# Performance work log

Measured on AMD Instinct MI355X. Metric: run time of the kernel, lower is better.

The kernel has to match this reference:

```python
import jax, jax.numpy as jnp
import numpy as np

N, NFEAT, NHID, NCLASS = 8192, 512, 256, 2
ALPHA = 0.5


def setup_inputs() -> dict:
    key = jax.random.key(0)
    k1, k2, k3, k4, k5 = jax.random.split(key, 5)
    x = jax.random.normal(k1, (N, NFEAT), dtype=jnp.float32)
    adj = jax.random.uniform(k2, (N, N), dtype=jnp.float32)
    # GraphConvolution init: uniform(-stdv, stdv), stdv = 1/sqrt(out_features)
    s1 = 1.0 / np.sqrt(NHID)
    W1 = jax.random.uniform(k3, (NFEAT, NHID), dtype=jnp.float32, minval=-s1, maxval=s1)
    s2 = 1.0 / np.sqrt(NCLASS)
    W2 = jax.random.uniform(k4, (NHID, NCLASS), dtype=jnp.float32, minval=-s2, maxval=s2)
    b2 = jax.random.uniform(k5, (NCLASS,), dtype=jnp.float32, minval=-s2, maxval=s2)
    return {"x": x, "adj": adj, "W1": W1, "W2": W2, "b2": b2}


def _mid_filter_2(adj, alpha):
    # D_row = diag(rowsum^-0.5), D_col = diag(colsum^-0.5); inf -> 0
    d_row = jnp.power(jnp.sum(adj, axis=1), -0.5)
    d_row = jnp.where(jnp.isinf(d_row), 0.0, d_row)
    d_col = jnp.power(jnp.sum(adj, axis=0), -0.5)
    d_col = jnp.where(jnp.isinf(d_col), 0.0, d_col)
    # (adj @ D_col)^T @ D_row)^T == d_row[:,None] * adj * d_col[None,:]
    DAD = d_row[:, None] * adj * d_col[None, :]
    I = jnp.eye(adj.shape[0], dtype=adj.dtype)
    return jnp.matmul(alpha * I - DAD, I + DAD)


def reference(x, adj, W1, W2, b2):
    adj_f = _mid_filter_2(adj, ALPHA)
    # hidden layer (no bias): relu(adj_f @ (x @ W1)); dropout = identity (eval)
    h = jax.nn.relu(jnp.matmul(adj_f, jnp.matmul(x, W1)))
    # output layer (with bias)
    out = jnp.matmul(adj_f, jnp.matmul(h, W2)) + b2
    return jax.nn.log_softmax(out, axis=-1)
```

## Files before the change

kernel.cpp:

```cpp
#include <hip/hip_runtime.h>
#include <hip/hip_bf16.h>

typedef unsigned short u16;
typedef unsigned int u32;
typedef __attribute__((ext_vector_type(8))) short short8;
typedef __attribute__((ext_vector_type(4))) float f32x4;

#define NN 8192
#define NF 512
#define NH 256
#define SPLITZ 4
#define RB 256

__device__ __forceinline__ float bf2f(u32 u) {
  union { u32 i; float f; } v; v.i = u << 16; return v.f;
}
__device__ __forceinline__ u16 f2bf(float f) {
  union { __hip_bfloat16 b; u16 u; } v; v.b = __float2bfloat16(f); return v.u;
}
__device__ __forceinline__ u32 pack2(float a, float b) {
  return (u32)f2bf(a) | ((u32)f2bf(b) << 16);
}

__global__ __launch_bounds__(256) void conv_adj_k(const float* __restrict__ adj,
                                                  u16* __restrict__ adjb,
                                                  float* __restrict__ rowsum_part,
                                                  float* __restrict__ colsum_part) {
  __shared__ float red[4][32];
  const int t = threadIdx.x;
  const int w = t >> 6, lane = t & 63;
  const int s = blockIdx.x;
  const int c0 = s * 2048 + t * 8;
  const int r0 = blockIdx.y * 32;
  float cp[8] = {0.f, 0.f, 0.f, 0.f, 0.f, 0.f, 0.f, 0.f};
  for (int r = 0; r < 32; ++r) {
    const size_t base = (size_t)(r0 + r) * NN + c0;
    float4 v0 = *(const float4*)(adj + base);
    float4 v1 = *(const float4*)(adj + base + 4);
    uint4 pk;
    pk.x = pack2(v0.x, v0.y); pk.y = pack2(v0.z, v0.w);
    pk.z = pack2(v1.x, v1.y); pk.w = pack2(v1.z, v1.w);
    *(uint4*)(adjb + base) = pk;
    cp[0] += v0.x; cp[1] += v0.y; cp[2] += v0.z; cp[3] += v0.w;
    cp[4] += v1.x; cp[5] += v1.y; cp[6] += v1.z; cp[7] += v1.w;
    float rs = (v0.x + v0.y) + (v0.z + v0.w) + ((v1.x + v1.y) + (v1.z + v1.w));
#pragma unroll
    for (int off = 32; off > 0; off >>= 1) rs += __shfl_down(rs, off, 64);
    if (lane == 0) red[w][r] = rs;
  }
  __syncthreads();
  if (t < 32)
    rowsum_part[(size_t)s * NN + r0 + t] =
        (red[0][t] + red[1][t]) + (red[2][t] + red[3][t]);
  float* cdst = colsum_part + (size_t)blockIdx.y * NN + c0;
  *(float4*)cdst = make_float4(cp[0], cp[1], cp[2], cp[3]);
  *(float4*)(cdst + 4) = make_float4(cp[4], cp[5], cp[6], cp[7]);
}

__global__ __launch_bounds__(256) void reduce_sums_k(const float* __restrict__ rowp,
                                                     const float* __restrict__ colp,
                                                     float* __restrict__ drow,
                                                     float* __restrict__ dcol) {
  const int i = blockIdx.x * 256 + threadIdx.x;
  const float rs = (rowp[i] + rowp[NN + i]) + (rowp[2 * NN + i] + rowp[3 * NN + i]);
  drow[i] = (rs > 0.f) ? rsqrtf(rs) : 0.f;
  float cs = 0.f;
#pragma unroll 8
  for (int rb = 0; rb < RB; ++rb) cs += colp[(size_t)rb * NN + i];
  dcol[i] = (cs > 0.f) ? rsqrtf(cs) : 0.f;
}

__global__ __launch_bounds__(256) void convx_k(const float* __restrict__ x,
                                               u16* __restrict__ xb) {
  const size_t i = ((size_t)blockIdx.x * 256 + threadIdx.x) * 8;
  float4 v0 = *(const float4*)(x + i);
  float4 v1 = *(const float4*)(x + i + 4);
  uint4 pk;
  pk.x = pack2(v0.x, v0.y); pk.y = pack2(v0.z, v0.w);
  pk.z = pack2(v1.x, v1.y); pk.w = pack2(v1.z, v1.w);
  *(uint4*)(xb + i) = pk;
}

__global__ __launch_bounds__(256) void convw1_k(const float* __restrict__ in,
                                                u16* __restrict__ out) {
  __shared__ float tile[32][33];
  const int tx = threadIdx.x & 31, ty = threadIdx.x >> 5;
  const int c0 = blockIdx.x * 32;
  const int r0 = blockIdx.y * 32;
#pragma unroll
  for (int d = 0; d < 32; d += 8)
    tile[ty + d][tx] = in[(size_t)(r0 + ty + d) * NH + c0 + tx];
  __syncthreads();
#pragma unroll
  for (int d = 0; d < 32; d += 8)
    out[(size_t)(c0 + ty + d) * NF + r0 + tx] = f2bf(tile[tx][ty + d]);
}

__device__ __forceinline__ void stage128(const u16* __restrict__ A, int lda,
                                         const u16* __restrict__ Bt, int ldb,
                                         int m0, int n0, int kk,
                                         u16* as_, u16* bs_, int tid) {
#pragma unroll
  for (int h = 0; h < 2; ++h) {
    const int slot = tid + h * 256;
    const int row = slot >> 2, kc = slot & 3;
    const u16* srcA = A + (size_t)(m0 + row) * lda + kk + kc * 8;
    __builtin_amdgcn_global_load_lds((const __attribute__((address_space(1))) void*)srcA,
                                     (__attribute__((address_space(3))) void*)(as_ + slot * 8),
                                     16, 0, 0);
    const u16* srcB = Bt + (size_t)(n0 + row) * ldb + kk + kc * 8;
    __builtin_amdgcn_global_load_lds((const __attribute__((address_space(1))) void*)srcB,
                                     (__attribute__((address_space(3))) void*)(bs_ + slot * 8),
                                     16, 0, 0);
  }
}

__global__ __launch_bounds__(256) void gemm_k(const u16* __restrict__ A, int lda,
                                              const u16* __restrict__ Bt, int ldb,
                                              int kChunk, float* __restrict__ out) {
  __shared__ __align__(16) u16 As[2][128 * 32];
  __shared__ __align__(16) u16 Bs[2][128 * 32];
  const int tid = threadIdx.x;
  const int w = tid >> 6, lane = tid & 63;
  const int lq = lane >> 4, lr = lane & 15;
  const int wr = (w >> 1) * 64, wc = (w & 1) * 64;
  const int n0 = blockIdx.x * 128;
  const int m0 = blockIdx.y * 128;
  const int kk0 = blockIdx.z * kChunk;
  const int nk = kChunk >> 5;

  f32x4 acc[4][4] = {};

  stage128(A, lda, Bt, ldb, m0, n0, kk0, As[0], Bs[0], tid);
  for (int kt = 0; kt < nk; ++kt) {
    const int cur = kt & 1;
    __syncthreads();
    if (kt + 1 < nk)
      stage128(A, lda, Bt, ldb, m0, n0, kk0 + ((kt + 1) << 5), As[cur ^ 1], Bs[cur ^ 1], tid);
    short8 a[4], b[4];
#pragma unroll
    for (int i = 0; i < 4; ++i)
      a[i] = *(const short8*)(As[cur] + (wr + i * 16 + lr) * 32 + lq * 8);
#pragma unroll
    for (int i = 0; i < 4; ++i)
      b[i] = *(const short8*)(Bs[cur] + (wc + i * 16 + lr) * 32 + lq * 8);
#pragma unroll
    for (int i = 0; i < 4; ++i)
#pragma unroll
      for (int j = 0; j < 4; ++j)
        acc[i][j] = __builtin_amdgcn_mfma_f32_16x16x32_bf16(a[i], b[j], acc[i][j], 0, 0, 0);
  }

  float* o = out + (size_t)blockIdx.z * ((size_t)NN * NH);
#pragma unroll
  for (int i = 0; i < 4; ++i)
#pragma unroll
    for (int j = 0; j < 4; ++j) {
      const int gn = n0 + wc + j * 16 + lr;
      const int gm0 = m0 + wr + i * 16 + lq * 4;
#pragma unroll
      for (int r = 0; r < 4; ++r)
        o[(size_t)(gm0 + r) * NH + gn] = acc[i][j][r];
    }
}

__global__ __launch_bounds__(256) void t1_k(const float* __restrict__ P,
                                            const float* __restrict__ dcol,
                                            u16* __restrict__ B1t) {
  __shared__ float tile[32][33];
  const int tx = threadIdx.x & 31, ty = threadIdx.x >> 5;
  const int c0 = blockIdx.x * 32;
  const int r0 = blockIdx.y * 32;
#pragma unroll
  for (int d = 0; d < 32; d += 8) {
    const int rr = r0 + ty + d;
    tile[ty + d][tx] = dcol[rr] * P[(size_t)rr * NH + c0 + tx];
  }
  __syncthreads();
#pragma unroll
  for (int d = 0; d < 32; d += 8)
    B1t[(size_t)(c0 + ty + d) * NN + r0 + tx] = f2bf(tile[tx][ty + d]);
}

__global__ __launch_bounds__(256) void r2_k(const float* __restrict__ Qp,
                                            const float* __restrict__ drow,
                                            const float* __restrict__ dcol,
                                            float* __restrict__ Q1,
                                            u16* __restrict__ B2t) {
  __shared__ float tile[32][33];
  const int tx = threadIdx.x & 31, ty = threadIdx.x >> 5;
  const int c0 = blockIdx.x * 32;
  const int r0 = blockIdx.y * 32;
  const size_t sl = (size_t)NN * NH;
#pragma unroll
  for (int d = 0; d < 32; d += 8) {
    const int rr = r0 + ty + d;
    const size_t idx = (size_t)rr * NH + c0 + tx;
    const float s = (Qp[idx] + Qp[idx + sl]) + (Qp[idx + 2 * sl] + Qp[idx + 3 * sl]);
    const float q = drow[rr] * s;
    Q1[idx] = q;
    tile[ty + d][tx] = dcol[rr] * q;
  }
  __syncthreads();
#pragma unroll
  for (int d = 0; d < 32; d += 8)
    B2t[(size_t)(c0 + ty + d) * NN + r0 + tx] = f2bf(tile[tx][ty + d]);
}

__global__ __launch_bounds__(256) void r3_k(const float* __restrict__ Hp,
                                            const float* __restrict__ P,
                                            const float* __restrict__ Q1,
                                            const float* __restrict__ drow,
                                            u16* __restrict__ Hb) {
  const size_t i = ((size_t)blockIdx.x * 256 + threadIdx.x) * 4;
  const int row = (int)(i >> 8);
  const size_t sl = (size_t)NN * NH;
  float4 a = *(const float4*)(Hp + i);
  float4 b = *(const float4*)(Hp + i + sl);
  float4 c = *(const float4*)(Hp + i + 2 * sl);
  float4 d = *(const float4*)(Hp + i + 3 * sl);
  float4 p = *(const float4*)(P + i);
  float4 q = *(const float4*)(Q1 + i);
  const float dr = drow[row];
  const float h0 = fmaxf(0.5f * p.x - 0.5f * q.x - dr * ((a.x + b.x) + (c.x + d.x)), 0.f);
  const float h1 = fmaxf(0.5f * p.y - 0.5f * q.y - dr * ((a.y + b.y) + (c.y + d.y)), 0.f);
  const float h2 = fmaxf(0.5f * p.z - 0.5f * q.z - dr * ((a.z + b.z) + (c.z + d.z)), 0.f);
  const float h3 = fmaxf(0.5f * p.w - 0.5f * q.w - dr * ((a.w + b.w) + (c.w + d.w)), 0.f);
  uint2 pk;
  pk.x = pack2(h0, h1);
  pk.y = pack2(h2, h3);
  *(uint2*)(Hb + i) = pk;
}

__global__ __launch_bounds__(256) void r_k(const u16* __restrict__ H,
                                           const float* __restrict__ W2,
                                           const float* __restrict__ dcol,
                                           float* __restrict__ R, float* __restrict__ B3) {
  const int w = threadIdx.x >> 6, lane = threadIdx.x & 63;
  const int i = blockIdx.x * 4 + w;
  uint2 hv = *(const uint2*)(H + (size_t)i * NH + lane * 4);
  float4 w01 = *(const float4*)(W2 + lane * 8);
  float4 w23 = *(const float4*)(W2 + lane * 8 + 4);
  const float h0 = bf2f(hv.x & 0xffffu), h1 = bf2f(hv.x >> 16);
  const float h2 = bf2f(hv.y & 0xffffu), h3 = bf2f(hv.y >> 16);
  float a0 = h0 * w01.x + h1 * w01.z + h2 * w23.x + h3 * w23.z;
  float a1 = h0 * w01.y + h1 * w01.w + h2 * w23.y + h3 * w23.w;
#pragma unroll
  for (int off = 32; off > 0; off >>= 1) {
    a0 += __shfl_down(a0, off, 64);
    a1 += __shfl_down(a1, off, 64);
  }
  if (lane == 0) {
    R[i * 2] = a0;
    R[i * 2 + 1] = a1;
    const float dc = dcol[i];
    B3[i * 2] = dc * a0;
    B3[i * 2 + 1] = dc * a1;
  }
}

__global__ __launch_bounds__(256) void gemv_k(
    const u16* __restrict__ adjb, const float* __restrict__ B,
    const float* __restrict__ drow, const float* __restrict__ dcol,
    const float* __restrict__ Rin, const float* __restrict__ S1in,
    const float* __restrict__ b2, float* __restrict__ S1out,
    float* __restrict__ B4, float* __restrict__ outp, int mode) {
  const int i = blockIdx.x;
  const int t = threadIdx.x;
  float a0 = 0.f, a1 = 0.f;
#pragma unroll
  for (int c = 0; c < 4; ++c) {
    const int col = c * 2048 + t * 8;
    uint4 av = *(const uint4*)(adjb + (size_t)i * NN + col);
    const u32* aw = (const u32*)&av;
    float bv[16];
    *(float4*)(bv) = *(const float4*)(B + col * 2);
    *(float4*)(bv + 4) = *(const float4*)(B + col * 2 + 4);
    *(float4*)(bv + 8) = *(const float4*)(B + col * 2 + 8);
    *(float4*)(bv + 12) = *(const float4*)(B + col * 2 + 12);
#pragma unroll
    for (int j = 0; j < 8; ++j) {
      const u32 a = aw[j >> 1];
      const float aval = bf2f((j & 1) ? (a >> 16) : (a & 0xffffu));
      a0 += aval * bv[2 * j];
      a1 += aval * bv[2 * j + 1];
    }
  }
#pragma unroll
  for (int off = 32; off > 0; off >>= 1) {
    a0 += __shfl_down(a0, off, 64);
    a1 += __shfl_down(a1, off, 64);
  }
  __shared__ float red[8];
  const int w = t >> 6, lane = t & 63;
  if (lane == 0) { red[w] = a0; red[4 + w] = a1; }
  __syncthreads();
  if (t == 0) {
    float s0 = (red[0] + red[1]) + (red[2] + red[3]);
    float s1 = (red[4] + red[5]) + (red[6] + red[7]);
    const float dr = drow[i];
    s0 *= dr; s1 *= dr;
    if (mode == 0) {
      S1out[i * 2] = s0;
      S1out[i * 2 + 1] = s1;
      const float dc = dcol[i];
      B4[i * 2] = dc * s0;
      B4[i * 2 + 1] = dc * s1;
    } else {
      const float l0 = 0.5f * Rin[i * 2] - 0.5f * S1in[i * 2] - s0 + b2[0];
      const float l1 = 0.5f * Rin[i * 2 + 1] - 0.5f * S1in[i * 2 + 1] - s1 + b2[1];
      const float m = fmaxf(l0, l1);
      const float lse = m + logf(__expf(l0 - m) + __expf(l1 - m));
      outp[i * 2] = l0 - lse;
      outp[i * 2 + 1] = l1 - lse;
    }
  }
}

extern "C" void kernel_launch(void* const* d_in, const int* in_sizes, int n_in,
                              void* d_out, int out_size, void* d_ws, size_t ws_size,
                              hipStream_t stream) {
  (void)in_sizes; (void)n_in; (void)out_size; (void)ws_size;
  const float* x   = (const float*)d_in[0];
  const float* adj = (const float*)d_in[1];
  const float* W1  = (const float*)d_in[2];
  const float* W2  = (const float*)d_in[3];
  const float* b2  = (const float*)d_in[4];
  float* outp = (float*)d_out;

  char* ws = (char*)d_ws;
  size_t off = 0;
  auto alloc = [&](size_t bytes) -> char* {
    char* p = ws + off;
    off += (bytes + 255) & ~(size_t)255;
    return p;
  };
  u16* adjb  = (u16*)alloc((size_t)NN * NN * 2);
  u16* xb    = (u16*)alloc((size_t)NN * NF * 2);
  u16* W1t   = (u16*)alloc((size_t)NH * NF * 2);
  float* rowp = (float*)alloc((size_t)4 * NN * 4);
  float* colp = (float*)alloc((size_t)RB * NN * 4);
  float* drow = (float*)alloc((size_t)NN * 4);
  float* dcol = (float*)alloc((size_t)NN * 4);
  float* P   = (float*)alloc((size_t)NN * NH * 4);
  u16* B1t   = (u16*)alloc((size_t)NH * NN * 2);
  float* Qp  = (float*)alloc((size_t)SPLITZ * NN * NH * 4);
  float* Q1  = (float*)alloc((size_t)NN * NH * 4);
  u16* B2t   = (u16*)alloc((size_t)NH * NN * 2);
  u16* Hb    = (u16*)alloc((size_t)NN * NH * 2);
  float* R   = (float*)alloc((size_t)NN * 2 * 4);
  float* B3  = (float*)alloc((size_t)NN * 2 * 4);
  float* S1  = (float*)alloc((size_t)NN * 2 * 4);
  float* B4  = (float*)alloc((size_t)NN * 2 * 4);
  float* Hp  = Qp;

  conv_adj_k<<<dim3(4, RB), 256, 0, stream>>>(adj, adjb, rowp, colp);
  reduce_sums_k<<<NN / 256, 256, 0, stream>>>(rowp, colp, drow, dcol);
  convx_k<<<2048, 256, 0, stream>>>(x, xb);
  convw1_k<<<dim3(8, 16), 256, 0, stream>>>(W1, W1t);

  gemm_k<<<dim3(2, 64, 1), 256, 0, stream>>>(xb, NF, W1t, NF, NF, P);
  t1_k<<<dim3(8, 256), 256, 0, stream>>>(P, dcol, B1t);

  gemm_k<<<dim3(2, 64, SPLITZ), 256, 0, stream>>>(adjb, NN, B1t, NN, NN / SPLITZ, Qp);
  r2_k<<<dim3(8, 256), 256, 0, stream>>>(Qp, drow, dcol, Q1, B2t);

  gemm_k<<<dim3(2, 64, SPLITZ), 256, 0, stream>>>(adjb, NN, B2t, NN, NN / SPLITZ, Hp);
  r3_k<<<2048, 256, 0, stream>>>(Hp, P, Q1, drow, Hb);

  r_k<<<NN / 4, 256, 0, stream>>>(Hb, W2, dcol, R, B3);
  gemv_k<<<NN, 256, 0, stream>>>(adjb, B3, drow, dcol, nullptr, nullptr, nullptr, S1, B4, nullptr, 0);
  gemv_k<<<NN, 256, 0, stream>>>(adjb, B4, drow, dcol, R, S1, b2, nullptr, nullptr, outp, 1);
}
```

Baseline: 661.7 us.

## Use 256x256-tile direct-to-LDS GEMM for adjacency products with deeper split-K

Replaces the two large adjacency GEMMs with a new 512-thread kernel whose 256x256 output tile spans the full hidden width. Each block reads its slice of the bf16 adjacency matrix once, instead of once per N-tile as before. The kernel stages A and B straight into double-buffered LDS with global_load_lds and uses 8x4 MFMA accumulators per wave. Split-K goes from 4 to 8 so the grid still fills the GPU, and the reduction kernels now loop over SPLITZ. The cost is twice as much partial-sum traffic, plus heavy LDS usage that limits occupancy and may cause bank conflicts.

```diff
diff --git a/kernel.cpp b/kernel.cpp
--- a/kernel.cpp
+++ b/kernel.cpp
@@ -9,7 +9,7 @@
 #define NN 8192
 #define NF 512
 #define NH 256
-#define SPLITZ 4
+#define SPLITZ 8
 #define RB 256
 
 __device__ __forceinline__ float bf2f(u32 u) {
@@ -164,6 +164,77 @@
     }
 }
 
+__device__ __forceinline__ void stage256(const u16* __restrict__ A, int lda,
+                                         const u16* __restrict__ Bt, int ldb,
+                                         int m0, int kk,
+                                         u16* as_, u16* bs_, int tid) {
+#pragma unroll
+  for (int h = 0; h < 4; ++h) {
+    const int slot = tid + h * 512;
+    const int row = slot >> 3, kc = (slot & 7) * 8;
+    const u16* srcA = A + (size_t)(m0 + row) * lda + kk + kc;
+    __builtin_amdgcn_global_load_lds((const __attribute__((address_space(1))) void*)srcA,
+                                     (__attribute__((address_space(3))) void*)(as_ + slot * 8),
+                                     16, 0, 0);
+    const u16* srcB = Bt + (size_t)row * ldb + kk + kc;
+    __builtin_amdgcn_global_load_lds((const __attribute__((address_space(1))) void*)srcB,
+                                     (__attribute__((address_space(3))) void*)(bs_ + slot * 8),
+                                     16, 0, 0);
+  }
+}
+
+__global__ __launch_bounds__(512, 2) void gemm256_k(const u16* __restrict__ A, int lda,
+                                                    const u16* __restrict__ Bt, int ldb,
+                                                    int kChunk, float* __restrict__ out) {
+  __shared__ __align__(16) u16 As[2][256 * 64];
+  __shared__ __align__(16) u16 Bs[2][256 * 64];
+  const int tid = threadIdx.x;
+  const int w = tid >> 6, lane = tid & 63;
+  const int lq = lane >> 4, lr = lane & 15;
+  const int wr = (w >> 2) * 128;
+  const int wc = (w & 3) * 64;
+  const int m0 = blockIdx.x * 256;
+  const int kk0 = blockIdx.y * kChunk;
+  const int nk = kChunk >> 6;
+
+  f32x4 acc[8][4] = {};
+
+  stage256(A, lda, Bt, ldb, m0, kk0, As[0], Bs[0], tid);
+  for (int kt = 0; kt < nk; ++kt) {
+    const int cur = kt & 1;
+    __syncthreads();
+    if (kt + 1 < nk)
+      stage256(A, lda, Bt, ldb, m0, kk0 + ((kt + 1) << 6), As[cur ^ 1], Bs[cur ^ 1], tid);
+#pragma unroll
+    for (int kk2 = 0; kk2 < 2; ++kk2) {
+      short8 a[8], b[4];
+#pragma unroll
+      for (int i = 0; i < 8; ++i)
+        a[i] = *(const short8*)(As[cur] + (wr + i * 16 + lr) * 64 + kk2 * 32 + lq * 8);
+#pragma unroll
+      for (int j = 0; j < 4; ++j)
+        b[j] = *(const short8*)(Bs[cur] + (wc + j * 16 + lr) * 64 + kk2 * 32 + lq * 8);
+#pragma unroll
+      for (int i = 0; i < 8; ++i)
+#pragma unroll
+        for (int j = 0; j < 4; ++j)
+          acc[i][j] = __builtin_amdgcn_mfma_f32_16x16x32_bf16(a[i], b[j], acc[i][j], 0, 0, 0);
+    }
+  }
+
+  float* o = out + (size_t)blockIdx.y * ((size_t)NN * NH);
+#pragma unroll
+  for (int i = 0; i < 8; ++i)
+#pragma unroll
+    for (int j = 0; j < 4; ++j) {
+      const int gn = wc + j * 16 + lr;
+      const int gm0 = m0 + wr + i * 16 + lq * 4;
+#pragma unroll
+      for (int r = 0; r < 4; ++r)
+        o[(size_t)(gm0 + r) * NH + gn] = acc[i][j][r];
+    }
+}
+
 __global__ __launch_bounds__(256) void t1_k(const float* __restrict__ P,
                                             const float* __restrict__ dcol,
                                             u16* __restrict__ B1t) {
@@ -196,7 +267,9 @@
   for (int d = 0; d < 32; d += 8) {
     const int rr = r0 + ty + d;
     const size_t idx = (size_t)rr * NH + c0 + tx;
-    const float s = (Qp[idx] + Qp[idx + sl]) + (Qp[idx + 2 * sl] + Qp[idx + 3 * sl]);
+    float s = 0.f;
+#pragma unroll
+    for (int z = 0; z < SPLITZ; ++z) s += Qp[idx + (size_t)z * sl];
     const float q = drow[rr] * s;
     Q1[idx] = q;
     tile[ty + d][tx] = dcol[rr] * q;
@@ -215,17 +288,19 @@
   const size_t i = ((size_t)blockIdx.x * 256 + threadIdx.x) * 4;
   const int row = (int)(i >> 8);
   const size_t sl = (size_t)NN * NH;
-  float4 a = *(const float4*)(Hp + i);
-  float4 b = *(const float4*)(Hp + i + sl);
-  float4 c = *(const float4*)(Hp + i + 2 * sl);
-  float4 d = *(const float4*)(Hp + i + 3 * sl);
+  float4 s = make_float4(0.f, 0.f, 0.f, 0.f);
+#pragma unroll
+  for (int z = 0; z < SPLITZ; ++z) {
+    float4 v = *(const float4*)(Hp + i + (size_t)z * sl);
+    s.x += v.x; s.y += v.y; s.z += v.z; s.w += v.w;
+  }
   float4 p = *(const float4*)(P + i);
   float4 q = *(const float4*)(Q1 + i);
   const float dr = drow[row];
-  const float h0 = fmaxf(0.5f * p.x - 0.5f * q.x - dr * ((a.x + b.x) + (c.x + d.x)), 0.f);
-  const float h1 = fmaxf(0.5f * p.y - 0.5f * q.y - dr * ((a.y + b.y) + (c.y + d.y)), 0.f);
-  const float h2 = fmaxf(0.5f * p.z - 0.5f * q.z - dr * ((a.z + b.z) + (c.z + d.z)), 0.f);
-  const float h3 = fmaxf(0.5f * p.w - 0.5f * q.w - dr * ((a.w + b.w) + (c.w + d.w)), 0.f);
+  const float h0 = fmaxf(0.5f * p.x - 0.5f * q.x - dr * s.x, 0.f);
+  const float h1 = fmaxf(0.5f * p.y - 0.5f * q.y - dr * s.y, 0.f);
+  const float h2 = fmaxf(0.5f * p.z - 0.5f * q.z - dr * s.z, 0.f);
+  const float h3 = fmaxf(0.5f * p.w - 0.5f * q.w - dr * s.w, 0.f);
   uint2 pk;
   pk.x = pack2(h0, h1);
   pk.y = pack2(h2, h3);
@@ -362,10 +437,10 @@
   gemm_k<<<dim3(2, 64, 1), 256, 0, stream>>>(xb, NF, W1t, NF, NF, P);
   t1_k<<<dim3(8, 256), 256, 0, stream>>>(P, dcol, B1t);
 
-  gemm_k<<<dim3(2, 64, SPLITZ), 256, 0, stream>>>(adjb, NN, B1t, NN, NN / SPLITZ, Qp);
+  gemm256_k<<<dim3(32, SPLITZ), 512, 0, stream>>>(adjb, NN, B1t, NN, NN / SPLITZ, Qp);
   r2_k<<<dim3(8, 256), 256, 0, stream>>>(Qp, drow, dcol, Q1, B2t);
 
-  gemm_k<<<dim3(2, 64, SPLITZ), 256, 0, stream>>>(adjb, NN, B2t, NN, NN / SPLITZ, Hp);
+  gemm256_k<<<dim3(32, SPLITZ), 512, 0, stream>>>(adjb, NN, B2t, NN, NN / SPLITZ, Hp);
   r3_k<<<2048, 256, 0, stream>>>(Hp, P, Q1, drow, Hb);
 
   r_k<<<NN / 4, 256, 0, stream>>>(Hb, W2, dcol, R, B3);
```

Result: no change. 652.8 us (-1.3%).

## Replace split-K adjacency GEMMs with full-N-width tile kernel and fuse epilogues

Applied to the files above, without the earlier changes.

Replaces the two split-K 8192x8192x256 adjacency GEMMs with a new kernel where each 512-thread block computes a 32x256 output strip over the whole K range. It uses double-buffered XOR-swizzled LDS tiles and applies the drow scaling in the epilogue, so the four-way partial-sum buffers and the reduction kernels r2_k and r3_k go away. The relu/H step is fused into the W2 projection kernel, and the x and W1 conversion kernels are merged into one launch. The risk is only 256 blocks with a small M tile, which may underfill the GPU and reuse adjacency tiles poorly compared with the 128x128 split-K tiling.

```diff
diff --git a/kernel.cpp b/kernel.cpp
--- a/kernel.cpp
+++ b/kernel.cpp
@@ -9,8 +9,8 @@
 #define NN 8192
 #define NF 512
 #define NH 256
-#define SPLITZ 4
 #define RB 256
+#define BKNZ 64
 
 __device__ __forceinline__ float bf2f(u32 u) {
   union { u32 i; float f; } v; v.i = u << 16; return v.f;
@@ -70,30 +70,32 @@
   dcol[i] = (cs > 0.f) ? rsqrtf(cs) : 0.f;
 }
 
-__global__ __launch_bounds__(256) void convx_k(const float* __restrict__ x,
-                                               u16* __restrict__ xb) {
-  const size_t i = ((size_t)blockIdx.x * 256 + threadIdx.x) * 8;
-  float4 v0 = *(const float4*)(x + i);
-  float4 v1 = *(const float4*)(x + i + 4);
-  uint4 pk;
-  pk.x = pack2(v0.x, v0.y); pk.y = pack2(v0.z, v0.w);
-  pk.z = pack2(v1.x, v1.y); pk.w = pack2(v1.z, v1.w);
-  *(uint4*)(xb + i) = pk;
-}
-
-__global__ __launch_bounds__(256) void convw1_k(const float* __restrict__ in,
-                                                u16* __restrict__ out) {
+__global__ __launch_bounds__(256) void convxw1_k(const float* __restrict__ x,
+                                                 u16* __restrict__ xb,
+                                                 const float* __restrict__ W1,
+                                                 u16* __restrict__ W1t) {
   __shared__ float tile[32][33];
-  const int tx = threadIdx.x & 31, ty = threadIdx.x >> 5;
-  const int c0 = blockIdx.x * 32;
-  const int r0 = blockIdx.y * 32;
-#pragma unroll
-  for (int d = 0; d < 32; d += 8)
-    tile[ty + d][tx] = in[(size_t)(r0 + ty + d) * NH + c0 + tx];
-  __syncthreads();
-#pragma unroll
-  for (int d = 0; d < 32; d += 8)
-    out[(size_t)(c0 + ty + d) * NF + r0 + tx] = f2bf(tile[tx][ty + d]);
+  if (blockIdx.x < 2048) {
+    const size_t i = ((size_t)blockIdx.x * 256 + threadIdx.x) * 8;
+    float4 v0 = *(const float4*)(x + i);
+    float4 v1 = *(const float4*)(x + i + 4);
+    uint4 pk;
+    pk.x = pack2(v0.x, v0.y); pk.y = pack2(v0.z, v0.w);
+    pk.z = pack2(v1.x, v1.y); pk.w = pack2(v1.z, v1.w);
+    *(uint4*)(xb + i) = pk;
+  } else {
+    const int blk = blockIdx.x - 2048;
+    const int tx = threadIdx.x & 31, ty = threadIdx.x >> 5;
+    const int c0 = (blk & 7) * 32;
+    const int r0 = (blk >> 3) * 32;
+#pragma unroll
+    for (int d = 0; d < 32; d += 8)
+      tile[ty + d][tx] = W1[(size_t)(r0 + ty + d) * NH + c0 + tx];
+    __syncthreads();
+#pragma unroll
+    for (int d = 0; d < 32; d += 8)
+      W1t[(size_t)(c0 + ty + d) * NF + r0 + tx] = f2bf(tile[tx][ty + d]);
+  }
 }
 
 __device__ __forceinline__ void stage128(const u16* __restrict__ A, int lda,
@@ -164,9 +166,89 @@
     }
 }
 
-__global__ __launch_bounds__(256) void t1_k(const float* __restrict__ P,
+__device__ __forceinline__ void stage_nz(const u16* __restrict__ A,
+                                         const u16* __restrict__ Bt,
+                                         int m0, int kk,
+                                         u16* as_, u16* bs_, int tid) {
+  if (tid < 256) {
+    const int row = tid >> 3, kc = (tid & 7) * 8;
+    const int sc = kc ^ ((row & 7) << 3);
+    const u16* srcA = A + (size_t)(m0 + row) * NN + kk + sc;
+    __builtin_amdgcn_global_load_lds((const __attribute__((address_space(1))) void*)srcA,
+                                     (__attribute__((address_space(3))) void*)(as_ + tid * 8),
+                                     16, 0, 0);
+  }
+#pragma unroll
+  for (int h = 0; h < 4; ++h) {
+    const int slot = tid + h * 512;
+    const int row = slot >> 3, kc = (slot & 7) * 8;
+    const int sc = kc ^ ((row & 7) << 3);
+    const u16* srcB = Bt + (size_t)row * NN + kk + sc;
+    __builtin_amdgcn_global_load_lds((const __attribute__((address_space(1))) void*)srcB,
+                                     (__attribute__((address_space(3))) void*)(bs_ + slot * 8),
+                                     16, 0, 0);
+  }
+}
+
+__global__ __launch_bounds__(512) void gemm_nz_k(const u16* __restrict__ A,
+                                                 const u16* __restrict__ Bt,
+                                                 const float* __restrict__ drow,
+                                                 float* __restrict__ out) {
+  __shared__ __align__(16) u16 As[2][32 * BKNZ];
+  __shared__ __align__(16) u16 Bs[2][256 * BKNZ];
+  const int tid = threadIdx.x;
+  const int w = tid >> 6, lane = tid & 63;
+  const int lq = lane >> 4, lr = lane & 15;
+  const int wc = w * 32;
+  const int m0 = blockIdx.x * 32;
+
+  f32x4 acc[2][2] = {};
+
+  stage_nz(A, Bt, m0, 0, As[0], Bs[0], tid);
+  const int nk = NN / BKNZ;
+  for (int kt = 0; kt < nk; ++kt) {
+    const int cur = kt & 1;
+    __syncthreads();
+    if (kt + 1 < nk)
+      stage_nz(A, Bt, m0, (kt + 1) * BKNZ, As[cur ^ 1], Bs[cur ^ 1], tid);
+#pragma unroll
+    for (int kk2 = 0; kk2 < BKNZ / 32; ++kk2) {
+      short8 a[2], b[2];
+#pragma unroll
+      for (int i = 0; i < 2; ++i) {
+        const int ar = i * 16 + lr;
+        const int sa = (kk2 * 32 + lq * 8) ^ ((ar & 7) << 3);
+        a[i] = *(const short8*)(As[cur] + ar * BKNZ + sa);
+      }
+#pragma unroll
+      for (int j = 0; j < 2; ++j) {
+        const int br = wc + j * 16 + lr;
+        const int sb = (kk2 * 32 + lq * 8) ^ ((br & 7) << 3);
+        b[j] = *(const short8*)(Bs[cur] + br * BKNZ + sb);
+      }
+#pragma unroll
+      for (int i = 0; i < 2; ++i)
+#pragma unroll
+        for (int j = 0; j < 2; ++j)
+          acc[i][j] = __builtin_amdgcn_mfma_f32_16x16x32_bf16(a[i], b[j], acc[i][j], 0, 0, 0);
+    }
+  }
+
+#pragma unroll
+  for (int i = 0; i < 2; ++i)
+#pragma unroll
+    for (int j = 0; j < 2; ++j) {
+      const int gn = wc + j * 16 + lr;
+      const int gm0 = m0 + i * 16 + lq * 4;
+#pragma unroll
+      for (int r = 0; r < 4; ++r)
+        out[(size_t)(gm0 + r) * NH + gn] = drow[gm0 + r] * acc[i][j][r];
+    }
+}
+
+__global__ __launch_bounds__(256) void t1_k(const float* __restrict__ S,
                                             const float* __restrict__ dcol,
-                                            u16* __restrict__ B1t) {
+                                            u16* __restrict__ Bt) {
   __shared__ float tile[32][33];
   const int tx = threadIdx.x & 31, ty = threadIdx.x >> 5;
   const int c0 = blockIdx.x * 32;
@@ -174,75 +256,33 @@
 #pragma unroll
   for (int d = 0; d < 32; d += 8) {
     const int rr = r0 + ty + d;
-    tile[ty + d][tx] = dcol[rr] * P[(size_t)rr * NH + c0 + tx];
+    tile[ty + d][tx] = dcol[rr] * S[(size_t)rr * NH + c0 + tx];
   }
   __syncthreads();
 #pragma unroll
   for (int d = 0; d < 32; d += 8)
-    B1t[(size_t)(c0 + ty + d) * NN + r0 + tx] = f2bf(tile[tx][ty + d]);
-}
-
-__global__ __launch_bounds__(256) void r2_k(const float* __restrict__ Qp,
-                                            const float* __restrict__ drow,
-                                            const float* __restrict__ dcol,
-                                            float* __restrict__ Q1,
-                                            u16* __restrict__ B2t) {
-  __shared__ float tile[32][33];
-  const int tx = threadIdx.x & 31, ty = threadIdx.x >> 5;
-  const int c0 = blockIdx.x * 32;
-  const int r0 = blockIdx.y * 32;
-  const size_t sl = (size_t)NN * NH;
-#pragma unroll
-  for (int d = 0; d < 32; d += 8) {
-    const int rr = r0 + ty + d;
-    const size_t idx = (size_t)rr * NH + c0 + tx;
-    const float s = (Qp[idx] + Qp[idx + sl]) + (Qp[idx + 2 * sl] + Qp[idx + 3 * sl]);
-    const float q = drow[rr] * s;
-    Q1[idx] = q;
-    tile[ty + d][tx] = dcol[rr] * q;
-  }
-  __syncthreads();
-#pragma unroll
-  for (int d = 0; d < 32; d += 8)
-    B2t[(size_t)(c0 + ty + d) * NN + r0 + tx] = f2bf(tile[tx][ty + d]);
-}
-
-__global__ __launch_bounds__(256) void r3_k(const float* __restrict__ Hp,
-                                            const float* __restrict__ P,
-                                            const float* __restrict__ Q1,
-                                            const float* __restrict__ drow,
-                                            u16* __restrict__ Hb) {
-  const size_t i = ((size_t)blockIdx.x * 256 + threadIdx.x) * 4;
-  const int row = (int)(i >> 8);
-  const size_t sl = (size_t)NN * NH;
-  float4 a = *(const float4*)(Hp + i);
-  float4 b = *(const float4*)(Hp + i + sl);
-  float4 c = *(const float4*)(Hp + i + 2 * sl);
-  float4 d = *(const float4*)(Hp + i + 3 * sl);
-  float4 p = *(const float4*)(P + i);
-  float4 q = *(const float4*)(Q1 + i);
-  const float dr = drow[row];
-  const float h0 = fmaxf(0.5f * p.x - 0.5f * q.x - dr * ((a.x + b.x) + (c.x + d.x)), 0.f);
-  const float h1 = fmaxf(0.5f * p.y - 0.5f * q.y - dr * ((a.y + b.y) + (c.y + d.y)), 0.f);
-  const float h2 = fmaxf(0.5f * p.z - 0.5f * q.z - dr * ((a.z + b.z) + (c.z + d.z)), 0.f);
-  const float h3 = fmaxf(0.5f * p.w - 0.5f * q.w - dr * ((a.w + b.w) + (c.w + d.w)), 0.f);
-  uint2 pk;
-  pk.x = pack2(h0, h1);
-  pk.y = pack2(h2, h3);
-  *(uint2*)(Hb + i) = pk;
-}
-
-__global__ __launch_bounds__(256) void r_k(const u16* __restrict__ H,
-                                           const float* __restrict__ W2,
-                                           const float* __restrict__ dcol,
-                                           float* __restrict__ R, float* __restrict__ B3) {
+    Bt[(size_t)(c0 + ty + d) * NN + r0 + tx] = f2bf(tile[tx][ty + d]);
+}
+
+__global__ __launch_bounds__(256) void r3r_k(const float* __restrict__ Hs,
+                                             const float* __restrict__ P,
+                                             const float* __restrict__ Q1,
+                                             const float* __restrict__ W2,
+                                             const float* __restrict__ dcol,
+                                             float* __restrict__ R,
+                                             float* __restrict__ B3) {
   const int w = threadIdx.x >> 6, lane = threadIdx.x & 63;
   const int i = blockIdx.x * 4 + w;
-  uint2 hv = *(const uint2*)(H + (size_t)i * NH + lane * 4);
+  const size_t base = (size_t)i * NH + lane * 4;
+  float4 p = *(const float4*)(P + base);
+  float4 q = *(const float4*)(Q1 + base);
+  float4 s = *(const float4*)(Hs + base);
+  const float h0 = fmaxf(0.5f * p.x - 0.5f * q.x - s.x, 0.f);
+  const float h1 = fmaxf(0.5f * p.y - 0.5f * q.y - s.y, 0.f);
+  const float h2 = fmaxf(0.5f * p.z - 0.5f * q.z - s.z, 0.f);
+  const float h3 = fmaxf(0.5f * p.w - 0.5f * q.w - s.w, 0.f);
   float4 w01 = *(const float4*)(W2 + lane * 8);
   float4 w23 = *(const float4*)(W2 + lane * 8 + 4);
-  const float h0 = bf2f(hv.x & 0xffffu), h1 = bf2f(hv.x >> 16);
-  const float h2 = bf2f(hv.y & 0xffffu), h3 = bf2f(hv.y >> 16);
   float a0 = h0 * w01.x + h1 * w01.z + h2 * w23.x + h3 * w23.z;
   float a1 = h0 * w01.y + h1 * w01.w + h2 * w23.y + h3 * w23.w;
 #pragma unroll
@@ -344,31 +384,28 @@
   float* dcol = (float*)alloc((size_t)NN * 4);
   float* P   = (float*)alloc((size_t)NN * NH * 4);
   u16* B1t   = (u16*)alloc((size_t)NH * NN * 2);
-  float* Qp  = (float*)alloc((size_t)SPLITZ * NN * NH * 4);
   float* Q1  = (float*)alloc((size_t)NN * NH * 4);
   u16* B2t   = (u16*)alloc((size_t)NH * NN * 2);
-  u16* Hb    = (u16*)alloc((size_t)NN * NH * 2);
+  float* Hs  = (float*)alloc((size_t)NN * NH * 4);
   float* R   = (float*)alloc((size_t)NN * 2 * 4);
   float* B3  = (float*)alloc((size_t)NN * 2 * 4);
   float* S1  = (float*)alloc((size_t)NN * 2 * 4);
   float* B4  = (float*)alloc((size_t)NN * 2 * 4);
-  float* Hp  = Qp;
 
   conv_adj_k<<<dim3(4, RB), 256, 0, stream>>>(adj, adjb, rowp, colp);
   reduce_sums_k<<<NN / 256, 256, 0, stream>>>(rowp, colp, drow, dcol);
-  convx_k<<<2048, 256, 0, stream>>>(x, xb);
-  convw1_k<<<dim3(8, 16), 256, 0, stream>>>(W1, W1t);
+  convxw1_k<<<2176, 256, 0, stream>>>(x, xb, W1, W1t);
 
   gemm_k<<<dim3(2, 64, 1), 256, 0, stream>>>(xb, NF, W1t, NF, NF, P);
   t1_k<<<dim3(8, 256), 256, 0, stream>>>(P, dcol, B1t);
 
-  gemm_k<<<dim3(2, 64, SPLITZ), 256, 0, stream>>>(adjb, NN, B1t, NN, NN / SPLITZ, Qp);
-  r2_k<<<dim3(8, 256), 256, 0, stream>>>(Qp, drow, dcol, Q1, B2t);
-
-  gemm_k<<<dim3(2, 64, SPLITZ), 256, 0, stream>>>(adjb, NN, B2t, NN, NN / SPLITZ, Hp);
-  r3_k<<<2048, 256, 0, stream>>>(Hp, P, Q1, drow, Hb);
-
-  r_k<<<NN / 4, 256, 0, stream>>>(Hb, W2, dcol, R, B3);
+  gemm_nz_k<<<256, 512, 0, stream>>>(adjb, B1t, drow, Q1);
+  t1_k<<<dim3(8, 256), 256, 0, stream>>>(Q1, dcol, B2t);
+
+  gemm_nz_k<<<256, 512, 0, stream>>>(adjb, B2t, drow, Hs);
+
+  r3r_k<<<NN / 4, 256, 0, stream>>>(Hs, P, Q1, W2, dcol, R, B3);
+
   gemv_k<<<NN, 256, 0, stream>>>(adjb, B3, drow, dcol, nullptr, nullptr, nullptr, S1, B4, nullptr, 0);
   gemv_k<<<NN, 256, 0, stream>>>(adjb, B4, drow, dcol, R, S1, b2, nullptr, nullptr, outp, 1);
 }
```

After: 749.8 us. 1.13x slower.
